# Performance work log

Hardware: AMD Instinct MI355X
Metric: run time of the kernel (lower is better)

Reference implementation:

```python
import jax, jax.numpy as jnp
import numpy as np

WINDOW_SIZE = 11
SIGMA = 1.5
MAX_VAL = 1.0


def _gaussian_kernel2d(ws: int, sigma: float) -> jnp.ndarray:
    # matches kornia gaussian_t: x = arange(ws) - ws//2, normalized 1D, outer product
    x = jnp.arange(ws, dtype=jnp.float32) - ws // 2
    g = jnp.exp(-(x * x) / (2.0 * sigma * sigma))
    g = g / g.sum()
    return jnp.outer(g, g)  # (ws, ws)


def _filter2d(x: jnp.ndarray, kernel: jnp.ndarray) -> jnp.ndarray:
    # depthwise 'same' conv with reflect padding, matching kornia filter2d
    B, C, H, W = x.shape
    kh, kw = kernel.shape
    pad_h = ((kh - 1) // 2, (kh - 1) - (kh - 1) // 2)
    pad_w = ((kw - 1) // 2, (kw - 1) - (kw - 1) // 2)
    xp = jnp.pad(x, ((0, 0), (0, 0), pad_h, pad_w), mode='reflect')
    k = jnp.broadcast_to(kernel[None, None], (C, 1, kh, kw)).astype(x.dtype)
    return jax.lax.conv_general_dilated(
        xp, k, window_strides=(1, 1), padding='VALID',
        dimension_numbers=('NCHW', 'OIHW', 'NCHW'), feature_group_count=C)


def setup_inputs() -> dict:
    key = jax.random.key(0)
    k1, k2 = jax.random.split(key)
    img1 = jax.random.uniform(k1, (16, 3, 512, 512), dtype=jnp.float32)
    img2 = jax.random.uniform(k2, (16, 3, 512, 512), dtype=jnp.float32)
    kernel = _gaussian_kernel2d(WINDOW_SIZE, SIGMA)  # fixed gaussian window (11,11)
    return {"img1": img1, "img2": img2, "kernel": kernel}


def reference(img1, img2, kernel):
    C1 = (0.01 * MAX_VAL) ** 2
    C2 = (0.03 * MAX_VAL) ** 2
    mu1 = _filter2d(img1, kernel)
    mu2 = _filter2d(img2, kernel)
    mu1_sq = mu1 * mu1
    mu2_sq = mu2 * mu2
    mu1_mu2 = mu1 * mu2
    sigma1_sq = _filter2d(img1 * img1, kernel) - mu1_sq
    sigma2_sq = _filter2d(img2 * img2, kernel) - mu2_sq
    sigma12 = _filter2d(img1 * img2, kernel) - mu1_mu2
    num = (2.0 * mu1_mu2 + C1) * (2.0 * sigma12 + C2)
    den = (mu1_sq + mu2_sq + C1) * (sigma1_sq + sigma2_sq + C2)
    return num / den  # (B, C, H, W) SSIM map ('same' padding -> no crop)
```

## Files before the change

kernel.cpp:

```cpp
#include <hip/hip_runtime.h>

namespace {

typedef __attribute__((ext_vector_type(2))) float f32x2;
typedef __attribute__((ext_vector_type(4))) float f32x4;

constexpr int Hd = 512, Wd = 512;
constexpr int TH = 32;
constexpr int R  = 4;
constexpr int NCH = TH / R;
constexpr int RAD = 5, WS = 11;
constexpr int HSTR = 524;
constexpr float C1c = 1e-4f;
constexpr float C2c = 9e-4f;

__device__ __forceinline__ float rcp_fast(float x) { return __builtin_amdgcn_rcpf(x); }
__device__ __forceinline__ float sgpr_f(float x) {
    return __int_as_float(__builtin_amdgcn_readfirstlane(__float_as_int(x)));
}

__global__ __launch_bounds__(512, 4) void ssim_map_kernel(
    const float* __restrict__ img1,
    const float* __restrict__ img2,
    const float* __restrict__ kern,
    float* __restrict__ out)
{
    __shared__ __align__(16) f32x2 hb01[R * HSTR];
    __shared__ __align__(16) f32x2 hb23[R * HSTR];
    __shared__ __align__(16) float hb4 [R * HSTR];

    const int tid  = threadIdx.x;
    const int c    = tid;
    const int row0 = blockIdx.x * TH;
    const long pbase = (long)blockIdx.y * (long)(Hd * Wd);

    float g[WS];
    {
        float s = 0.f;
#pragma unroll
        for (int j = 0; j < WS; ++j) s += kern[RAD * WS + j];
        const float inv = 1.0f / s;
#pragma unroll
        for (int j = 0; j < WS; ++j) g[j] = sgpr_f(kern[RAD * WS + j] * inv);
    }

    f32x2 aV[WS], aE[WS];
    float aP[WS];
#pragma unroll
    for (int i = 0; i < WS; ++i) {
        aV[i].x = 0.f; aV[i].y = 0.f;
        aE[i].x = 0.f; aE[i].y = 0.f;
        aP[i] = 0.f;
    }

#pragma unroll
    for (int j = 0; j < 2 * RAD; ++j) {
        int gr = row0 - RAD + j;
        gr = (gr < 0) ? -gr : gr;
        gr = (gr >= Hd) ? (2 * Hd - 2 - gr) : gr;
        const long off = pbase + (long)gr * Wd + c;
        const float a = img1[off];
        const float b = img2[off];
        f32x2 ab; ab.x = a; ab.y = b;
        const f32x2 pp = ab * ab;
        const float p12 = a * b;
#pragma unroll
        for (int k = 0; k < WS; ++k) {
            if (k <= j) {
                const int slot = (j - k) % WS;
                f32x2 w2; w2.x = g[k]; w2.y = g[k];
                aV[slot] = __builtin_elementwise_fma(w2, ab, aV[slot]);
                aE[slot] = __builtin_elementwise_fma(w2, pp, aE[slot]);
                aP[slot] = fmaf(g[k], p12, aP[slot]);
            }
        }
    }

    const int hr = tid >> 7;
    const int hu = tid & 127;

#pragma unroll
    for (int ch = 0; ch < NCH; ++ch) {
        __syncthreads();

#pragma unroll
        for (int i = 0; i < R; ++i) {
            const int o = ch * R + i;
            const int j = o + 2 * RAD;
            int gr = row0 - RAD + j;
            gr = (gr < 0) ? -gr : gr;
            gr = (gr >= Hd) ? (2 * Hd - 2 - gr) : gr;
            const long off = pbase + (long)gr * Wd + c;
            const float a = img1[off];
            const float b = img2[off];
            f32x2 ab; ab.x = a; ab.y = b;
            const f32x2 pp = ab * ab;
            const float p12 = a * b;
#pragma unroll
            for (int k = 0; k < WS; ++k) {
                const int slot = (j - k) % WS;
                f32x2 w2; w2.x = g[k]; w2.y = g[k];
                aV[slot] = __builtin_elementwise_fma(w2, ab, aV[slot]);
                aE[slot] = __builtin_elementwise_fma(w2, pp, aE[slot]);
                aP[slot] = fmaf(g[k], p12, aP[slot]);
            }
            const int es = o % WS;
            hb01[i * HSTR + RAD + c] = aV[es];
            hb23[i * HSTR + RAD + c] = aE[es];
            hb4 [i * HSTR + RAD + c] = aP[es];
            if (c >= 1 && c <= RAD) {
                hb01[i * HSTR + RAD - c] = aV[es];
                hb23[i * HSTR + RAD - c] = aE[es];
                hb4 [i * HSTR + RAD - c] = aP[es];
            } else if (c >= Wd - 1 - RAD && c <= Wd - 2) {
                hb01[i * HSTR + RAD + 1022 - c] = aV[es];
                hb23[i * HSTR + RAD + 1022 - c] = aE[es];
                hb4 [i * HSTR + RAD + 1022 - c] = aP[es];
            }
            aV[es].x = 0.f; aV[es].y = 0.f;
            aE[es].x = 0.f; aE[es].y = 0.f;
            aP[es] = 0.f;
        }

        __syncthreads();

        f32x2 h01[4], h23[4];
        float h4[4];
        {
            const f32x4* p4 = (const f32x4*)&hb01[hr * HSTR + 4 * hu];
            f32x2 f[14];
#pragma unroll
            for (int i = 0; i < 7; ++i) {
                const f32x4 t = p4[i];
                f[2*i] = t.lo; f[2*i+1] = t.hi;
            }
#pragma unroll
            for (int j = 0; j < 4; ++j) { h01[j].x = 0.f; h01[j].y = 0.f; }
#pragma unroll
            for (int k = 0; k < WS; ++k) {
                f32x2 w2; w2.x = g[k]; w2.y = g[k];
#pragma unroll
                for (int j = 0; j < 4; ++j)
                    h01[j] = __builtin_elementwise_fma(w2, f[k + j], h01[j]);
            }
        }
        {
            const f32x4* p4 = (const f32x4*)&hb23[hr * HSTR + 4 * hu];
            f32x2 f[14];
#pragma unroll
            for (int i = 0; i < 7; ++i) {
                const f32x4 t = p4[i];
                f[2*i] = t.lo; f[2*i+1] = t.hi;
            }
#pragma unroll
            for (int j = 0; j < 4; ++j) { h23[j].x = 0.f; h23[j].y = 0.f; }
#pragma unroll
            for (int k = 0; k < WS; ++k) {
                f32x2 w2; w2.x = g[k]; w2.y = g[k];
#pragma unroll
                for (int j = 0; j < 4; ++j)
                    h23[j] = __builtin_elementwise_fma(w2, f[k + j], h23[j]);
            }
        }
        {
            const float* base = &hb4[hr * HSTR + 4 * hu];
            const f32x4 v0 = *(const f32x4*)(base);
            const f32x4 v1 = *(const f32x4*)(base + 4);
            const f32x4 v2 = *(const f32x4*)(base + 8);
            const f32x2 v3 = *(const f32x2*)(base + 12);
            const float f[14] = { v0.x, v0.y, v0.z, v0.w,
                                  v1.x, v1.y, v1.z, v1.w,
                                  v2.x, v2.y, v2.z, v2.w,
                                  v3.x, v3.y };
#pragma unroll
            for (int j = 0; j < 4; ++j) h4[j] = 0.f;
#pragma unroll
            for (int k = 0; k < WS; ++k) {
#pragma unroll
                for (int j = 0; j < 4; ++j)
                    h4[j] = fmaf(g[k], f[k + j], h4[j]);
            }
        }

        float rr[4];
#pragma unroll
        for (int j = 0; j < 4; ++j) {
            const f32x2 mm  = h01[j];
            const f32x2 msq = mm * mm;
            const f32x2 sg  = h23[j] - msq;
            const float m12  = mm.x * mm.y;
            const float sg12 = h4[j] - m12;
            const float num = (2.f * m12 + C1c) * (2.f * sg12 + C2c);
            const float den = (msq.x + msq.y + C1c) * (sg.x + sg.y + C2c);
            rr[j] = num * rcp_fast(den);
        }
        f32x4 res; res.x = rr[0]; res.y = rr[1]; res.z = rr[2]; res.w = rr[3];
        f32x4* po = (f32x4*)&out[pbase + (long)(row0 + ch * R + hr) * Wd + 4 * hu];
        *po = res;
    }
}

}

extern "C" void kernel_launch(void* const* d_in, const int* in_sizes, int n_in,
                              void* d_out, int out_size, void* d_ws, size_t ws_size,
                              hipStream_t stream) {
    const float* img1 = (const float*)d_in[0];
    const float* img2 = (const float*)d_in[1];
    const float* kern = (const float*)d_in[2];
    float* outp = (float*)d_out;
    dim3 grid(Hd / TH, 48);
    ssim_map_kernel<<<grid, dim3(512), 0, stream>>>(img1, img2, kern, outp);
}
```

Before: 172.6 us.

## Filter sum/difference channels to reduce five blurred quantities to four

Rewrites SSIM in terms of s=a+b and d=a-b, so only four quantities are blurred (mean and mean-square of s and d) instead of five (two means, two second moments, cross product). This cuts the vertical and horizontal FMA count and shared-memory traffic by about a fifth, and packs the four channels into one f32x4 shared buffer with a single vectorized store per pixel. The horizontal pass is restructured to stream 14 float4 loads and raise launch-bounds occupancy to 6. The reformulation subtracts nearly equal large quantities, so it risks extra float32 cancellation error in the variance terms, and the higher occupancy target may force register spills.

```diff
diff --git a/kernel.cpp b/kernel.cpp
--- a/kernel.cpp
+++ b/kernel.cpp
@@ -19,15 +19,13 @@
     return __int_as_float(__builtin_amdgcn_readfirstlane(__float_as_int(x)));
 }
 
-__global__ __launch_bounds__(512, 4) void ssim_map_kernel(
+__global__ __launch_bounds__(512, 6) void ssim_map_kernel(
     const float* __restrict__ img1,
     const float* __restrict__ img2,
     const float* __restrict__ kern,
     float* __restrict__ out)
 {
-    __shared__ __align__(16) f32x2 hb01[R * HSTR];
-    __shared__ __align__(16) f32x2 hb23[R * HSTR];
-    __shared__ __align__(16) float hb4 [R * HSTR];
+    __shared__ __align__(16) f32x4 hb[R * HSTR];
 
     const int tid  = threadIdx.x;
     const int c    = tid;
@@ -44,13 +42,12 @@
         for (int j = 0; j < WS; ++j) g[j] = sgpr_f(kern[RAD * WS + j] * inv);
     }
 
-    f32x2 aV[WS], aE[WS];
-    float aP[WS];
+    f32x2 aM[WS];
+    f32x2 aQ[WS];
 #pragma unroll
     for (int i = 0; i < WS; ++i) {
-        aV[i].x = 0.f; aV[i].y = 0.f;
-        aE[i].x = 0.f; aE[i].y = 0.f;
-        aP[i] = 0.f;
+        aM[i].x = 0.f; aM[i].y = 0.f;
+        aQ[i].x = 0.f; aQ[i].y = 0.f;
     }
 
 #pragma unroll
@@ -61,17 +58,15 @@
         const long off = pbase + (long)gr * Wd + c;
         const float a = img1[off];
         const float b = img2[off];
-        f32x2 ab; ab.x = a; ab.y = b;
-        const f32x2 pp = ab * ab;
-        const float p12 = a * b;
+        f32x2 sd; sd.x = a + b; sd.y = a - b;
+        const f32x2 qq = sd * sd;
 #pragma unroll
         for (int k = 0; k < WS; ++k) {
             if (k <= j) {
                 const int slot = (j - k) % WS;
                 f32x2 w2; w2.x = g[k]; w2.y = g[k];
-                aV[slot] = __builtin_elementwise_fma(w2, ab, aV[slot]);
-                aE[slot] = __builtin_elementwise_fma(w2, pp, aE[slot]);
-                aP[slot] = fmaf(g[k], p12, aP[slot]);
+                aM[slot] = __builtin_elementwise_fma(w2, sd, aM[slot]);
+                aQ[slot] = __builtin_elementwise_fma(w2, qq, aQ[slot]);
             }
         }
     }
@@ -93,105 +88,66 @@
             const long off = pbase + (long)gr * Wd + c;
             const float a = img1[off];
             const float b = img2[off];
-            f32x2 ab; ab.x = a; ab.y = b;
-            const f32x2 pp = ab * ab;
-            const float p12 = a * b;
+            f32x2 sd; sd.x = a + b; sd.y = a - b;
+            const f32x2 qq = sd * sd;
 #pragma unroll
             for (int k = 0; k < WS; ++k) {
                 const int slot = (j - k) % WS;
                 f32x2 w2; w2.x = g[k]; w2.y = g[k];
-                aV[slot] = __builtin_elementwise_fma(w2, ab, aV[slot]);
-                aE[slot] = __builtin_elementwise_fma(w2, pp, aE[slot]);
-                aP[slot] = fmaf(g[k], p12, aP[slot]);
+                aM[slot] = __builtin_elementwise_fma(w2, sd, aM[slot]);
+                aQ[slot] = __builtin_elementwise_fma(w2, qq, aQ[slot]);
             }
             const int es = o % WS;
-            hb01[i * HSTR + RAD + c] = aV[es];
-            hb23[i * HSTR + RAD + c] = aE[es];
-            hb4 [i * HSTR + RAD + c] = aP[es];
+            f32x4 e;
+            e.x = aM[es].x; e.y = aM[es].y;
+            e.z = aQ[es].x; e.w = aQ[es].y;
+            hb[i * HSTR + RAD + c] = e;
             if (c >= 1 && c <= RAD) {
-                hb01[i * HSTR + RAD - c] = aV[es];
-                hb23[i * HSTR + RAD - c] = aE[es];
-                hb4 [i * HSTR + RAD - c] = aP[es];
+                hb[i * HSTR + RAD - c] = e;
             } else if (c >= Wd - 1 - RAD && c <= Wd - 2) {
-                hb01[i * HSTR + RAD + 1022 - c] = aV[es];
-                hb23[i * HSTR + RAD + 1022 - c] = aE[es];
-                hb4 [i * HSTR + RAD + 1022 - c] = aP[es];
+                hb[i * HSTR + RAD + 1022 - c] = e;
             }
-            aV[es].x = 0.f; aV[es].y = 0.f;
-            aE[es].x = 0.f; aE[es].y = 0.f;
-            aP[es] = 0.f;
+            aM[es].x = 0.f; aM[es].y = 0.f;
+            aQ[es].x = 0.f; aQ[es].y = 0.f;
         }
 
         __syncthreads();
 
-        f32x2 h01[4], h23[4];
-        float h4[4];
-        {
-            const f32x4* p4 = (const f32x4*)&hb01[hr * HSTR + 4 * hu];
-            f32x2 f[14];
+        f32x2 hm[4], hq[4];
 #pragma unroll
-            for (int i = 0; i < 7; ++i) {
-                const f32x4 t = p4[i];
-                f[2*i] = t.lo; f[2*i+1] = t.hi;
-            }
+        for (int j = 0; j < 4; ++j) {
+            hm[j].x = 0.f; hm[j].y = 0.f;
+            hq[j].x = 0.f; hq[j].y = 0.f;
+        }
+        const f32x4* base = &hb[hr * HSTR + 4 * hu];
 #pragma unroll
-            for (int j = 0; j < 4; ++j) { h01[j].x = 0.f; h01[j].y = 0.f; }
+        for (int t = 0; t < 14; ++t) {
+            const f32x4 ft = base[t];
+            f32x2 fm; fm.x = ft.x; fm.y = ft.y;
+            f32x2 fq; fq.x = ft.z; fq.y = ft.w;
 #pragma unroll
-            for (int k = 0; k < WS; ++k) {
-                f32x2 w2; w2.x = g[k]; w2.y = g[k];
-#pragma unroll
-                for (int j = 0; j < 4; ++j)
-                    h01[j] = __builtin_elementwise_fma(w2, f[k + j], h01[j]);
-            }
-        }
-        {
-            const f32x4* p4 = (const f32x4*)&hb23[hr * HSTR + 4 * hu];
-            f32x2 f[14];
-#pragma unroll
-            for (int i = 0; i < 7; ++i) {
-                const f32x4 t = p4[i];
-                f[2*i] = t.lo; f[2*i+1] = t.hi;
-            }
-#pragma unroll
-            for (int j = 0; j < 4; ++j) { h23[j].x = 0.f; h23[j].y = 0.f; }
-#pragma unroll
-            for (int k = 0; k < WS; ++k) {
-                f32x2 w2; w2.x = g[k]; w2.y = g[k];
-#pragma unroll
-                for (int j = 0; j < 4; ++j)
-                    h23[j] = __builtin_elementwise_fma(w2, f[k + j], h23[j]);
-            }
-        }
-        {
-            const float* base = &hb4[hr * HSTR + 4 * hu];
-            const f32x4 v0 = *(const f32x4*)(base);
-            const f32x4 v1 = *(const f32x4*)(base + 4);
-            const f32x4 v2 = *(const f32x4*)(base + 8);
-            const f32x2 v3 = *(const f32x2*)(base + 12);
-            const float f[14] = { v0.x, v0.y, v0.z, v0.w,
-                                  v1.x, v1.y, v1.z, v1.w,
-                                  v2.x, v2.y, v2.z, v2.w,
-                                  v3.x, v3.y };
-#pragma unroll
-            for (int j = 0; j < 4; ++j) h4[j] = 0.f;
-#pragma unroll
-            for (int k = 0; k < WS; ++k) {
-#pragma unroll
-                for (int j = 0; j < 4; ++j)
-                    h4[j] = fmaf(g[k], f[k + j], h4[j]);
+            for (int j = 0; j < 4; ++j) {
+                const int k = t - j;
+                if (k >= 0 && k < WS) {
+                    f32x2 w2; w2.x = g[k]; w2.y = g[k];
+                    hm[j] = __builtin_elementwise_fma(w2, fm, hm[j]);
+                    hq[j] = __builtin_elementwise_fma(w2, fq, hq[j]);
+                }
             }
         }
 
         float rr[4];
 #pragma unroll
         for (int j = 0; j < 4; ++j) {
-            const f32x2 mm  = h01[j];
-            const f32x2 msq = mm * mm;
-            const f32x2 sg  = h23[j] - msq;
-            const float m12  = mm.x * mm.y;
-            const float sg12 = h4[j] - m12;
-            const float num = (2.f * m12 + C1c) * (2.f * sg12 + C2c);
-            const float den = (msq.x + msq.y + C1c) * (sg.x + sg.y + C2c);
+            const f32x2 m = hm[j];
+            const f32x2 q = hq[j];
+            const f32x2 msq = m * m;
+            const float t1 = msq.x - msq.y;
+            const float t2 = msq.x + msq.y;
+            const float q1 = q.x - q.y;
+            const float q2 = q.x + q.y;
+            const float num = fmaf(0.5f, t1, C1c) * fmaf(0.5f, q1 - t1, C2c);
+            const float den = fmaf(0.5f, t2, C1c) * fmaf(0.5f, q2 - t2, C2c);
             rr[j] = num * rcp_fast(den);
         }
         f32x4 res; res.x = rr[0]; res.y = rr[1]; res.z = rr[2]; res.w = rr[3];
```

New measurement: 161.9 us. 6.2% less time.
